# Kernel optimization log

Hardware: AMD Instinct MI355X
Metric: run time of the kernel (lower is better)

Reference implementation:

```python
import jax, jax.numpy as jnp
import numpy as np

B, S, HID = 2, 2048, 2048
H, KV, D = 16, 8, 128
EPS = 1e-6


def _rope_embeds(B, S, D):
    # standard RoPE cos/sin table, concatenated along last dim: [B, S, D]
    pos = jnp.arange(S, dtype=jnp.float32)  # same positions per batch row
    inv_freq = 1.0 / (10000.0 ** (jnp.arange(0, D // 2, dtype=jnp.float32) * (2.0 / D)))
    ang = pos[:, None] * inv_freq[None, :]  # [S, D/2]
    pe = jnp.concatenate([jnp.cos(ang), jnp.sin(ang)], axis=-1)  # [S, D]
    return jnp.broadcast_to(pe[None], (B, S, D))


def setup_inputs() -> dict:
    key = jax.random.key(0)
    ks = jax.random.split(key, 5)
    scale = 0.02
    return {
        "x": jax.random.normal(ks[0], (B, S, HID), jnp.float32),
        "pos_embeds": _rope_embeds(B, S, D),
        "q_w": jax.random.normal(ks[1], (H * D, HID), jnp.float32) * scale,
        "k_w": jax.random.normal(ks[2], (KV * D, HID), jnp.float32) * scale,
        "v_w": jax.random.normal(ks[3], (KV * D, HID), jnp.float32) * scale,
        "o_w": jax.random.normal(ks[4], (HID, H * D), jnp.float32) * scale,
        "q_norm_w": jnp.ones((D,), jnp.float32),
        "k_norm_w": jnp.ones((D,), jnp.float32),
    }


def _rmsnorm(x, w):
    var = jnp.mean(jnp.square(x), axis=-1, keepdims=True)
    return x * jax.lax.rsqrt(var + EPS) * w


def _apply_rope(x, pos_embeds):
    # x: [B, S, h, D]; pos_embeds: [B, S, D] = cat(cos, sin)
    x1, x2 = jnp.split(x, 2, axis=-1)
    cos, sin = jnp.split(pos_embeds[:, :, None, :], 2, axis=-1)
    return jnp.concatenate([x1 * cos - x2 * sin, x1 * sin + x2 * cos], axis=-1)


def reference(x, pos_embeds, q_w, k_w, v_w, o_w, q_norm_w, k_norm_w):
    b, s, _ = x.shape
    q = _apply_rope(_rmsnorm((x @ q_w.T).reshape(b, s, H, D), q_norm_w), pos_embeds)
    k = _apply_rope(_rmsnorm((x @ k_w.T).reshape(b, s, KV, D), k_norm_w), pos_embeds)
    v = (x @ v_w.T).reshape(b, s, KV, D)
    # GQA: repeat kv heads to match query heads
    rep = H // KV
    k = jnp.repeat(k, rep, axis=2)
    v = jnp.repeat(v, rep, axis=2)
    scores = jnp.einsum("bqhd,bkhd->bhqk", q, k) * (1.0 / np.sqrt(D))
    causal = jnp.tril(jnp.ones((s, s), dtype=bool))
    scores = jnp.where(causal[None, None], scores, jnp.finfo(scores.dtype).min)
    attn = jax.nn.softmax(scores, axis=-1)
    out = jnp.einsum("bhqk,bkhd->bqhd", attn, v).reshape(b, s, H * D)
    return out @ o_w.T
```

## Files before the change

### kernel.cpp

```cpp
#include <hip/hip_runtime.h>
#include <hip/hip_bf16.h>

#define BATCH 2
#define SEQ   2048
#define HID   2048
#define NH    16
#define NKV   8
#define HD    128

typedef __bf16 bf16;
typedef bf16  bf16x8  __attribute__((ext_vector_type(8)));
typedef bf16  bf16x4  __attribute__((ext_vector_type(4)));
typedef float floatx4 __attribute__((ext_vector_type(4)));

typedef __attribute__((address_space(3))) void lds_void;
typedef const __attribute__((address_space(1))) void gmem_void;

__device__ inline void async16(const void* g, void* l) {
    __builtin_amdgcn_global_load_lds((gmem_void*)g, (lds_void*)l, 16, 0, 0);
}

#define XN  8388608u
#define QWN 4194304u
#define KWN 2097152u
#define VWN 2097152u
#define OWN 4194304u

__global__ __launch_bounds__(256) void cvt_all(bf16* __restrict__ dst,
                                               const float* __restrict__ x,
                                               const float* __restrict__ qw,
                                               const float* __restrict__ kw,
                                               const float* __restrict__ vw,
                                               const float* __restrict__ ow)
{
    const int blk = blockIdx.x;
    const float* src;
    size_t off;
    if (blk < 4096)      { src = x;  off = (size_t)blk * 2048; }
    else if (blk < 6144) { src = qw; off = (size_t)(blk - 4096) * 2048; }
    else if (blk < 7168) { src = kw; off = (size_t)(blk - 6144) * 2048; }
    else if (blk < 8192) { src = vw; off = (size_t)(blk - 7168) * 2048; }
    else                 { src = ow; off = (size_t)(blk - 8192) * 2048; }

    const int t = threadIdx.x * 8;
    const float4* p = (const float4*)(src + off + t);
    float4 u0 = p[0], u1 = p[1];
    bf16x8 v;
    v[0] = (bf16)u0.x; v[1] = (bf16)u0.y; v[2] = (bf16)u0.z; v[3] = (bf16)u0.w;
    v[4] = (bf16)u1.x; v[5] = (bf16)u1.y; v[6] = (bf16)u1.z; v[7] = (bf16)u1.w;
    *(bf16x8*)(dst + (size_t)blk * 2048 + t) = v;
}

template <int AMODE, int WMODE, int CMODE>
__global__ __launch_bounds__(256) void gemm128(void* __restrict__ Cp,
                                               const void* __restrict__ Ap,
                                               const void* __restrict__ Wp,
                                               int M, int N, int K)
{
    __shared__ bf16 As[128 * 64];
    __shared__ bf16 Ws[128 * 64];

    const int tid  = threadIdx.x;
    const int wv   = tid >> 6;
    const int lane = tid & 63;
    const int quad = lane >> 4;
    const int c    = lane & 15;

    const int m0 = blockIdx.x * 128;
    const int n0 = blockIdx.y * 128;
    const int wm = (wv >> 1) * 64;
    const int wn = (wv & 1) * 64;

    const int arow = lane >> 3;
    const int acol = (lane & 7) * 8;

    floatx4 acc[4][4] = {};

    for (int k0 = 0; k0 < K; k0 += 64) {
        if constexpr (AMODE == 0) {
            const float* A = (const float*)Ap;
            #pragma unroll
            for (int it = 0; it < 4; it++) {
                int row = it * 32 + (tid >> 3);
                int col = (tid & 7) * 8;
                const float4* p = (const float4*)(A + (size_t)(m0 + row) * K + k0 + col);
                float4 u0 = p[0], u1 = p[1];
                bf16x8 v;
                v[0] = (bf16)u0.x; v[1] = (bf16)u0.y; v[2] = (bf16)u0.z; v[3] = (bf16)u0.w;
                v[4] = (bf16)u1.x; v[5] = (bf16)u1.y; v[6] = (bf16)u1.z; v[7] = (bf16)u1.w;
                *(bf16x8*)(&As[row * 64 + col]) = v;
            }
        } else {
            const bf16* A = (const bf16*)Ap;
            #pragma unroll
            for (int ch = 0; ch < 4; ch++) {
                int row = wv * 32 + ch * 8 + arow;
                async16(A + (size_t)(m0 + row) * K + k0 + acol,
                        &As[(wv * 32 + ch * 8) * 64]);
            }
        }
        if constexpr (WMODE == 0) {
            const float* W = (const float*)Wp;
            #pragma unroll
            for (int it = 0; it < 4; it++) {
                int row = it * 32 + (tid >> 3);
                int col = (tid & 7) * 8;
                const float4* p = (const float4*)(W + (size_t)(n0 + row) * K + k0 + col);
                float4 u0 = p[0], u1 = p[1];
                bf16x8 v;
                v[0] = (bf16)u0.x; v[1] = (bf16)u0.y; v[2] = (bf16)u0.z; v[3] = (bf16)u0.w;
                v[4] = (bf16)u1.x; v[5] = (bf16)u1.y; v[6] = (bf16)u1.z; v[7] = (bf16)u1.w;
                *(bf16x8*)(&Ws[row * 64 + col]) = v;
            }
        } else {
            const bf16* W = (const bf16*)Wp;
            #pragma unroll
            for (int ch = 0; ch < 4; ch++) {
                int row = wv * 32 + ch * 8 + arow;
                async16(W + (size_t)(n0 + row) * K + k0 + acol,
                        &Ws[(wv * 32 + ch * 8) * 64]);
            }
        }
        __syncthreads();

        #pragma unroll
        for (int t = 0; t < 2; t++) {
            bf16x8 af[4], bw[4];
            #pragma unroll
            for (int i = 0; i < 4; i++)
                af[i] = *(const bf16x8*)(&As[(wm + i * 16 + c) * 64 + t * 32 + quad * 8]);
            #pragma unroll
            for (int j = 0; j < 4; j++)
                bw[j] = *(const bf16x8*)(&Ws[(wn + j * 16 + c) * 64 + t * 32 + quad * 8]);
            #pragma unroll
            for (int i = 0; i < 4; i++)
                #pragma unroll
                for (int j = 0; j < 4; j++)
                    acc[i][j] = __builtin_amdgcn_mfma_f32_16x16x32_bf16(af[i], bw[j], acc[i][j], 0, 0, 0);
        }
        __syncthreads();
    }

    if constexpr (CMODE == 0) {
        float* C = (float*)Cp;
        #pragma unroll
        for (int i = 0; i < 4; i++)
            #pragma unroll
            for (int j = 0; j < 4; j++)
                #pragma unroll
                for (int r = 0; r < 4; r++) {
                    int m = m0 + wm + i * 16 + quad * 4 + r;
                    int n = n0 + wn + j * 16 + c;
                    C[(size_t)m * N + n] = acc[i][j][r];
                }
    } else if constexpr (CMODE == 1) {
        bf16* C = (bf16*)Cp;
        #pragma unroll
        for (int i = 0; i < 4; i++)
            #pragma unroll
            for (int j = 0; j < 4; j++)
                #pragma unroll
                for (int r = 0; r < 4; r++) {
                    int m = m0 + wm + i * 16 + quad * 4 + r;
                    int n = n0 + wn + j * 16 + c;
                    C[(size_t)m * N + n] = (bf16)acc[i][j][r];
                }
    } else if constexpr (CMODE == 2) {
        bf16* C = (bf16*)Cp;
        const int b = m0 >> 11;
        #pragma unroll
        for (int j = 0; j < 4; j++) {
            int n = n0 + wn + j * 16 + c;
            size_t base = ((size_t)b * N + n) * 2048;
            #pragma unroll
            for (int i = 0; i < 4; i++) {
                int s0 = (m0 & 2047) + wm + i * 16 + quad * 4;
                bf16x4 v;
                #pragma unroll
                for (int r = 0; r < 4; r++) v[r] = (bf16)acc[i][j][r];
                *(bf16x4*)(&C[base + s0]) = v;
            }
        }
    } else {
        bf16* Cq = (bf16*)Cp;
        if (n0 < 2048) {
            #pragma unroll
            for (int i = 0; i < 4; i++)
                #pragma unroll
                for (int j = 0; j < 4; j++)
                    #pragma unroll
                    for (int r = 0; r < 4; r++) {
                        int m = m0 + wm + i * 16 + quad * 4 + r;
                        int n = n0 + wn + j * 16 + c;
                        Cq[(size_t)m * 2048 + n] = (bf16)acc[i][j][r];
                    }
        } else if (n0 < 3072) {
            bf16* Ck = Cq + XN;
            #pragma unroll
            for (int i = 0; i < 4; i++)
                #pragma unroll
                for (int j = 0; j < 4; j++)
                    #pragma unroll
                    for (int r = 0; r < 4; r++) {
                        int m = m0 + wm + i * 16 + quad * 4 + r;
                        int n = n0 - 2048 + wn + j * 16 + c;
                        Ck[(size_t)m * 1024 + n] = (bf16)acc[i][j][r];
                    }
        } else {
            bf16* Cv = Cq + XN + QWN;
            const int b = m0 >> 11;
            #pragma unroll
            for (int j = 0; j < 4; j++) {
                int n = n0 - 3072 + wn + j * 16 + c;
                size_t base = ((size_t)b * 1024 + n) * 2048;
                #pragma unroll
                for (int i = 0; i < 4; i++) {
                    int s0 = (m0 & 2047) + wm + i * 16 + quad * 4;
                    bf16x4 v;
                    #pragma unroll
                    for (int r = 0; r < 4; r++) v[r] = (bf16)acc[i][j][r];
                    *(bf16x4*)(&Cv[base + s0]) = v;
                }
            }
        }
    }
}

__global__ __launch_bounds__(256) void gemm_o64(float* __restrict__ C,
                                                const bf16* __restrict__ A,
                                                const bf16* __restrict__ W,
                                                int M, int N, int K)
{
    __shared__ bf16 As[128 * 64];
    __shared__ bf16 Ws[64 * 64];

    const int tid  = threadIdx.x;
    const int wv   = tid >> 6;
    const int lane = tid & 63;
    const int quad = lane >> 4;
    const int c    = lane & 15;

    const int m0 = blockIdx.x * 128;
    const int n0 = blockIdx.y * 64;
    const int wm = (wv >> 1) * 64;
    const int wn = (wv & 1) * 32;

    const int arow = lane >> 3;
    const int acol = (lane & 7) * 8;

    floatx4 acc[4][2] = {};

    for (int k0 = 0; k0 < K; k0 += 64) {
        #pragma unroll
        for (int ch = 0; ch < 4; ch++) {
            int row = wv * 32 + ch * 8 + arow;
            async16(A + (size_t)(m0 + row) * K + k0 + acol,
                    &As[(wv * 32 + ch * 8) * 64]);
        }
        #pragma unroll
        for (int ch = 0; ch < 2; ch++) {
            int row = wv * 16 + ch * 8 + arow;
            async16(W + (size_t)(n0 + row) * K + k0 + acol,
                    &Ws[(wv * 16 + ch * 8) * 64]);
        }
        __syncthreads();

        #pragma unroll
        for (int t = 0; t < 2; t++) {
            bf16x8 af[4], bw[2];
            #pragma unroll
            for (int i = 0; i < 4; i++)
                af[i] = *(const bf16x8*)(&As[(wm + i * 16 + c) * 64 + t * 32 + quad * 8]);
            #pragma unroll
            for (int j = 0; j < 2; j++)
                bw[j] = *(const bf16x8*)(&Ws[(wn + j * 16 + c) * 64 + t * 32 + quad * 8]);
            #pragma unroll
            for (int i = 0; i < 4; i++)
                #pragma unroll
                for (int j = 0; j < 2; j++)
                    acc[i][j] = __builtin_amdgcn_mfma_f32_16x16x32_bf16(af[i], bw[j], acc[i][j], 0, 0, 0);
        }
        __syncthreads();
    }

    #pragma unroll
    for (int i = 0; i < 4; i++)
        #pragma unroll
        for (int j = 0; j < 2; j++)
            #pragma unroll
            for (int r = 0; r < 4; r++) {
                int m = m0 + wm + i * 16 + quad * 4 + r;
                int n = n0 + wn + j * 16 + c;
                C[(size_t)m * N + n] = acc[i][j][r];
            }
}

__global__ __launch_bounds__(128) void norm_rope_k(bf16* __restrict__ k,
                                                   const float* __restrict__ pe,
                                                   const float* __restrict__ knw)
{
    const int s  = blockIdx.x;
    const int hh = blockIdx.y;
    const int b  = blockIdx.z;
    const int d  = threadIdx.x;

    bf16* buf = k + (size_t)(b * SEQ + s) * 1024 + hh * HD;

    float x = (float)buf[d];
    float ss = x * x;
    #pragma unroll
    for (int m = 32; m; m >>= 1) ss += __shfl_xor(ss, m);

    __shared__ float red[2];
    __shared__ float nv[128];
    if ((d & 63) == 0) red[d >> 6] = ss;
    __syncthreads();
    float var = (red[0] + red[1]) * (1.0f / 128.0f);
    float nx = x * rsqrtf(var + 1e-6f) * knw[d];
    nv[d] = nx;
    __syncthreads();

    const float* pev = pe + ((size_t)b * SEQ + s) * HD;
    float o;
    if (d < 64) {
        o = nx * pev[d] - nv[d + 64] * pev[64 + d];
    } else {
        o = nv[d - 64] * pev[d] + nx * pev[d - 64];
    }
    buf[d] = (bf16)o;
}

__global__ __launch_bounds__(256) void fattn(bf16* __restrict__ O,
                                             const bf16* __restrict__ Q,
                                             const bf16* __restrict__ Kh,
                                             const bf16* __restrict__ Vtg,
                                             const float* __restrict__ pe,
                                             const float* __restrict__ qnw)
{
    const int h    = blockIdx.y;
    const int b    = blockIdx.z;
    const int qblk = (h & 8) ? (int)blockIdx.x
                             : ((int)gridDim.x - 1 - (int)blockIdx.x);
    const int kv   = h >> 1;

    const int tid  = threadIdx.x;
    const int wv   = tid >> 6;
    const int lane = tid & 63;
    const int quad = lane >> 4;
    const int c    = lane & 15;

    __shared__ bf16 Ks[64 * 136];
    __shared__ bf16 Vs[128 * 72];
    __shared__ bf16 Ps[4 * 16 * 72];

    const int qw = qblk * 64 + wv * 16;

    bf16x8 qf[4];
    {
        const bf16* qp = Q + (size_t)(b * SEQ + qw + c) * 2048 + h * HD + quad * 8;
        float qv[4][8];
        float ss = 0.0f;
        #pragma unroll
        for (int t = 0; t < 4; t++) {
            bf16x8 raw = *(const bf16x8*)(qp + t * 32);
            #pragma unroll
            for (int j = 0; j < 8; j++) { qv[t][j] = (float)raw[j]; ss += qv[t][j] * qv[t][j]; }
        }
        ss += __shfl_xor(ss, 16);
        ss += __shfl_xor(ss, 32);
        const float inv = rsqrtf(ss * (1.0f / 128.0f) + 1e-6f);
        const float* pev = pe + (size_t)(b * SEQ + qw + c) * HD + quad * 8;
        float nx[4][8], pv[4][8];
        #pragma unroll
        for (int t = 0; t < 4; t++)
            #pragma unroll
            for (int j = 0; j < 8; j++) {
                pv[t][j] = pev[t * 32 + j];
                nx[t][j] = qv[t][j] * inv * qnw[t * 32 + quad * 8 + j];
            }
        #pragma unroll
        for (int t = 0; t < 2; t++)
            #pragma unroll
            for (int j = 0; j < 8; j++) {
                qf[t][j]     = (bf16)(nx[t][j] * pv[t][j]     - nx[t + 2][j] * pv[t + 2][j]);
                qf[t + 2][j] = (bf16)(nx[t][j] * pv[t + 2][j] + nx[t + 2][j] * pv[t][j]);
            }
    }

    floatx4 o_acc[8] = {};
    float l_part[4] = {};

    const bf16* kbase = Kh  + (size_t)b * SEQ * 1024 + kv * HD;
    const bf16* vbase = Vtg + ((size_t)b * 1024 + kv * HD) * 2048;

    const int kr  = tid >> 2, ksc = (tid & 3) * 32;
    const int vd  = tid >> 1, vkc = (tid & 1) * 32;
    bf16* psw = &Ps[wv * 16 * 72];
    const int nkt = qblk + 1;
    const float kS = 0.08838834764831845f * 1.4426950408889634f;
    const float kB = 11.5f * 1.4426950408889634f;

    bf16x8 kreg[4], vreg[4];
    {
        const bf16* kp = kbase + (size_t)kr * 1024 + ksc;
        const bf16* vp = vbase + (size_t)vd * 2048 + vkc;
        #pragma unroll
        for (int i = 0; i < 4; i++) kreg[i] = *(const bf16x8*)(kp + i * 8);
        #pragma unroll
        for (int i = 0; i < 4; i++) vreg[i] = *(const bf16x8*)(vp + i * 8);
    }

    for (int kt = 0; kt < nkt; kt++) {
        const int k0 = kt * 64;
        #pragma unroll
        for (int i = 0; i < 4; i++)
            *(bf16x8*)(&Ks[kr * 136 + ksc + i * 8]) = kreg[i];
        #pragma unroll
        for (int i = 0; i < 4; i++)
            *(bf16x8*)(&Vs[vd * 72 + vkc + i * 8]) = vreg[i];
        __syncthreads();

        if (kt + 1 < nkt) {
            const bf16* kp = kbase + (size_t)(k0 + 64 + kr) * 1024 + ksc;
            const bf16* vp = vbase + (size_t)vd * 2048 + (k0 + 64) + vkc;
            #pragma unroll
            for (int i = 0; i < 4; i++) kreg[i] = *(const bf16x8*)(kp + i * 8);
            #pragma unroll
            for (int i = 0; i < 4; i++) vreg[i] = *(const bf16x8*)(vp + i * 8);
        }

        floatx4 sc[4] = {};
        #pragma unroll
        for (int t = 0; t < 4; t++) {
            #pragma unroll
            for (int g = 0; g < 4; g++) {
                bf16x8 kf = *(const bf16x8*)(&Ks[(g * 16 + c) * 136 + t * 32 + quad * 8]);
                sc[g] = __builtin_amdgcn_mfma_f32_16x16x32_bf16(qf[t], kf, sc[g], 0, 0, 0);
            }
        }

        const bool last = (kt == nkt - 1);
        #pragma unroll
        for (int r = 0; r < 4; r++) {
            const int qrow = qw + quad * 4 + r;
            #pragma unroll
            for (int g = 0; g < 4; g++) {
                float p = exp2f(sc[g][r] * kS - kB);
                if (last && (k0 + g * 16 + c > qrow)) p = 0.0f;
                l_part[r] += p;
                psw[(quad * 4 + r) * 72 + g * 16 + c] = (bf16)p;
            }
        }
        asm volatile("s_waitcnt lgkmcnt(0)" ::: "memory");
        bf16x8 pf0 = *(const bf16x8*)(&psw[c * 72 + quad * 8]);
        bf16x8 pf1 = *(const bf16x8*)(&psw[c * 72 + 32 + quad * 8]);

        #pragma unroll
        for (int f = 0; f < 8; f++) {
            bf16x8 vf0 = *(const bf16x8*)(&Vs[(f * 16 + c) * 72 + quad * 8]);
            bf16x8 vf1 = *(const bf16x8*)(&Vs[(f * 16 + c) * 72 + 32 + quad * 8]);
            o_acc[f] = __builtin_amdgcn_mfma_f32_16x16x32_bf16(pf0, vf0, o_acc[f], 0, 0, 0);
            o_acc[f] = __builtin_amdgcn_mfma_f32_16x16x32_bf16(pf1, vf1, o_acc[f], 0, 0, 0);
        }
        __syncthreads();
    }

    #pragma unroll
    for (int r = 0; r < 4; r++) {
        float l = l_part[r];
        #pragma unroll
        for (int msk = 8; msk; msk >>= 1) l += __shfl_xor(l, msk);
        const float inv = 1.0f / l;
        bf16* op = O + (size_t)(b * SEQ + qw + quad * 4 + r) * 2048 + h * HD;
        #pragma unroll
        for (int f = 0; f < 8; f++) op[f * 16 + c] = (bf16)(o_acc[f][r] * inv);
    }
}

extern "C" void kernel_launch(void* const* d_in, const int* in_sizes, int n_in,
                              void* d_out, int out_size, void* d_ws, size_t ws_size,
                              hipStream_t stream)
{
    const float* x   = (const float*)d_in[0];
    const float* pe  = (const float*)d_in[1];
    const float* qw  = (const float*)d_in[2];
    const float* kw  = (const float*)d_in[3];
    const float* vw  = (const float*)d_in[4];
    const float* ow  = (const float*)d_in[5];
    const float* qnw = (const float*)d_in[6];
    const float* knw = (const float*)d_in[7];
    float* out = (float*)d_out;

    bf16* qb = (bf16*)d_ws;
    bf16* kb = qb + XN;
    bf16* vt = kb + KWN * 2;
    bf16* ab = vt + VWN * 2;
    bf16* cvt_base = ab + XN;

    const bool fit = ws_size >= (size_t)92274688;
    const int M = BATCH * SEQ;

    if (fit) {
        bf16* xb  = cvt_base;
        bf16* qwb = xb  + XN;
        bf16* owb = qwb + QWN + KWN + VWN;

        cvt_all<<<10240, 256, 0, stream>>>(xb, x, qw, kw, vw, ow);

        gemm128<1, 1, 3><<<dim3(32, 32), 256, 0, stream>>>(qb, xb, qwb, M, 4096, 2048);

        norm_rope_k<<<dim3(SEQ, NKV, BATCH), 128, 0, stream>>>(kb, pe, knw);
        fattn<<<dim3(SEQ / 64, NH, BATCH), 256, 0, stream>>>(ab, qb, kb, vt, pe, qnw);

        gemm_o64<<<dim3(32, 32), 256, 0, stream>>>(out, ab, owb, M, 2048, 2048);
    } else {
        gemm128<0, 0, 1><<<dim3(32, 16), 256, 0, stream>>>(qb, x, qw, M, 2048, 2048);
        gemm128<0, 0, 1><<<dim3(32,  8), 256, 0, stream>>>(kb, x, kw, M, 1024, 2048);
        gemm128<0, 0, 2><<<dim3(32,  8), 256, 0, stream>>>(vt, x, vw, M, 1024, 2048);

        norm_rope_k<<<dim3(SEQ, NKV, BATCH), 128, 0, stream>>>(kb, pe, knw);
        fattn<<<dim3(SEQ / 64, NH, BATCH), 256, 0, stream>>>(ab, qb, kb, vt, pe, qnw);

        gemm128<0, 0, 0><<<dim3(32, 16), 256, 0, stream>>>(out, ab, ow, M, 2048, 2048);
    }
}
```

Baseline: 402.5 us.

## Process 128 query rows per attention block to reuse K/V tiles

Each attention workgroup now covers 128 query rows instead of 64, with every wave handling two 16-row query sub-blocks against the same K/V tiles staged in LDS. This halves the number of K/V tile loads per query row and doubles the MFMA work per synchronisation. The P scratch buffer is resized with a padded stride, and causal masking is applied over the last two key tiles. The cost is higher register pressure from doubled accumulators, possibly lower occupancy, half as many workgroups, and more wasted masked work in the diagonal tiles.

```diff
diff --git a/kernel.cpp b/kernel.cpp
--- a/kernel.cpp
+++ b/kernel.cpp
@@ -351,13 +351,14 @@
 
     __shared__ bf16 Ks[64 * 136];
     __shared__ bf16 Vs[128 * 72];
-    __shared__ bf16 Ps[4 * 16 * 72];
-
-    const int qw = qblk * 64 + wv * 16;
-
-    bf16x8 qf[4];
-    {
-        const bf16* qp = Q + (size_t)(b * SEQ + qw + c) * 2048 + h * HD + quad * 8;
+    __shared__ bf16 Ps[4 * 32 * 76];
+
+    const int qw = qblk * 128 + wv * 32;
+
+    bf16x8 qf[2][4];
+    #pragma unroll
+    for (int ib = 0; ib < 2; ib++) {
+        const bf16* qp = Q + (size_t)(b * SEQ + qw + ib * 16 + c) * 2048 + h * HD + quad * 8;
         float qv[4][8];
         float ss = 0.0f;
         #pragma unroll
@@ -369,7 +370,7 @@
         ss += __shfl_xor(ss, 16);
         ss += __shfl_xor(ss, 32);
         const float inv = rsqrtf(ss * (1.0f / 128.0f) + 1e-6f);
-        const float* pev = pe + (size_t)(b * SEQ + qw + c) * HD + quad * 8;
+        const float* pev = pe + (size_t)(b * SEQ + qw + ib * 16 + c) * HD + quad * 8;
         float nx[4][8], pv[4][8];
         #pragma unroll
         for (int t = 0; t < 4; t++)
@@ -382,21 +383,21 @@
         for (int t = 0; t < 2; t++)
             #pragma unroll
             for (int j = 0; j < 8; j++) {
-                qf[t][j]     = (bf16)(nx[t][j] * pv[t][j]     - nx[t + 2][j] * pv[t + 2][j]);
-                qf[t + 2][j] = (bf16)(nx[t][j] * pv[t + 2][j] + nx[t + 2][j] * pv[t][j]);
-            }
-    }
-
-    floatx4 o_acc[8] = {};
-    float l_part[4] = {};
+                qf[ib][t][j]     = (bf16)(nx[t][j] * pv[t][j]     - nx[t + 2][j] * pv[t + 2][j]);
+                qf[ib][t + 2][j] = (bf16)(nx[t][j] * pv[t + 2][j] + nx[t + 2][j] * pv[t][j]);
+            }
+    }
+
+    floatx4 o_acc[2][8] = {};
+    float l_part[2][4] = {};
 
     const bf16* kbase = Kh  + (size_t)b * SEQ * 1024 + kv * HD;
     const bf16* vbase = Vtg + ((size_t)b * 1024 + kv * HD) * 2048;
 
     const int kr  = tid >> 2, ksc = (tid & 3) * 32;
     const int vd  = tid >> 1, vkc = (tid & 1) * 32;
-    bf16* psw = &Ps[wv * 16 * 72];
-    const int nkt = qblk + 1;
+    bf16* psw = &Ps[wv * 32 * 76];
+    const int nkt = 2 * qblk + 2;
     const float kS = 0.08838834764831845f * 1.4426950408889634f;
     const float kB = 11.5f * 1.4426950408889634f;
 
@@ -429,51 +430,67 @@
             for (int i = 0; i < 4; i++) vreg[i] = *(const bf16x8*)(vp + i * 8);
         }
 
-        floatx4 sc[4] = {};
+        floatx4 sc0[4] = {}, sc1[4] = {};
         #pragma unroll
         for (int t = 0; t < 4; t++) {
             #pragma unroll
             for (int g = 0; g < 4; g++) {
                 bf16x8 kf = *(const bf16x8*)(&Ks[(g * 16 + c) * 136 + t * 32 + quad * 8]);
-                sc[g] = __builtin_amdgcn_mfma_f32_16x16x32_bf16(qf[t], kf, sc[g], 0, 0, 0);
-            }
-        }
-
-        const bool last = (kt == nkt - 1);
+                sc0[g] = __builtin_amdgcn_mfma_f32_16x16x32_bf16(qf[0][t], kf, sc0[g], 0, 0, 0);
+                sc1[g] = __builtin_amdgcn_mfma_f32_16x16x32_bf16(qf[1][t], kf, sc1[g], 0, 0, 0);
+            }
+        }
+
+        const bool tail = (kt >= nkt - 2);
         #pragma unroll
         for (int r = 0; r < 4; r++) {
-            const int qrow = qw + quad * 4 + r;
+            const int qrow0 = qw + quad * 4 + r;
+            const int qrow1 = qrow0 + 16;
             #pragma unroll
             for (int g = 0; g < 4; g++) {
-                float p = exp2f(sc[g][r] * kS - kB);
-                if (last && (k0 + g * 16 + c > qrow)) p = 0.0f;
-                l_part[r] += p;
-                psw[(quad * 4 + r) * 72 + g * 16 + c] = (bf16)p;
+                float p0 = exp2f(sc0[g][r] * kS - kB);
+                float p1 = exp2f(sc1[g][r] * kS - kB);
+                if (tail) {
+                    const int key = k0 + g * 16 + c;
+                    if (key > qrow0) p0 = 0.0f;
+                    if (key > qrow1) p1 = 0.0f;
+                }
+                l_part[0][r] += p0;
+                l_part[1][r] += p1;
+                psw[(quad * 4 + r) * 76 + g * 16 + c]        = (bf16)p0;
+                psw[(16 + quad * 4 + r) * 76 + g * 16 + c]   = (bf16)p1;
             }
         }
         asm volatile("s_waitcnt lgkmcnt(0)" ::: "memory");
-        bf16x8 pf0 = *(const bf16x8*)(&psw[c * 72 + quad * 8]);
-        bf16x8 pf1 = *(const bf16x8*)(&psw[c * 72 + 32 + quad * 8]);
+        bf16x8 pf00 = *(const bf16x8*)(&psw[c * 76 + quad * 8]);
+        bf16x8 pf01 = *(const bf16x8*)(&psw[c * 76 + 32 + quad * 8]);
+        bf16x8 pf10 = *(const bf16x8*)(&psw[(16 + c) * 76 + quad * 8]);
+        bf16x8 pf11 = *(const bf16x8*)(&psw[(16 + c) * 76 + 32 + quad * 8]);
 
         #pragma unroll
         for (int f = 0; f < 8; f++) {
             bf16x8 vf0 = *(const bf16x8*)(&Vs[(f * 16 + c) * 72 + quad * 8]);
             bf16x8 vf1 = *(const bf16x8*)(&Vs[(f * 16 + c) * 72 + 32 + quad * 8]);
-            o_acc[f] = __builtin_amdgcn_mfma_f32_16x16x32_bf16(pf0, vf0, o_acc[f], 0, 0, 0);
-            o_acc[f] = __builtin_amdgcn_mfma_f32_16x16x32_bf16(pf1, vf1, o_acc[f], 0, 0, 0);
+            o_acc[0][f] = __builtin_amdgcn_mfma_f32_16x16x32_bf16(pf00, vf0, o_acc[0][f], 0, 0, 0);
+            o_acc[0][f] = __builtin_amdgcn_mfma_f32_16x16x32_bf16(pf01, vf1, o_acc[0][f], 0, 0, 0);
+            o_acc[1][f] = __builtin_amdgcn_mfma_f32_16x16x32_bf16(pf10, vf0, o_acc[1][f], 0, 0, 0);
+            o_acc[1][f] = __builtin_amdgcn_mfma_f32_16x16x32_bf16(pf11, vf1, o_acc[1][f], 0, 0, 0);
         }
         __syncthreads();
     }
 
     #pragma unroll
-    for (int r = 0; r < 4; r++) {
-        float l = l_part[r];
-        #pragma unroll
-        for (int msk = 8; msk; msk >>= 1) l += __shfl_xor(l, msk);
-        const float inv = 1.0f / l;
-        bf16* op = O + (size_t)(b * SEQ + qw + quad * 4 + r) * 2048 + h * HD;
-        #pragma unroll
-        for (int f = 0; f < 8; f++) op[f * 16 + c] = (bf16)(o_acc[f][r] * inv);
+    for (int ib = 0; ib < 2; ib++) {
+        #pragma unroll
+        for (int r = 0; r < 4; r++) {
+            float l = l_part[ib][r];
+            #pragma unroll
+            for (int msk = 8; msk; msk >>= 1) l += __shfl_xor(l, msk);
+            const float inv = 1.0f / l;
+            bf16* op = O + (size_t)(b * SEQ + qw + ib * 16 + quad * 4 + r) * 2048 + h * HD;
+            #pragma unroll
+            for (int f = 0; f < 8; f++) op[f * 16 + c] = (bf16)(o_acc[ib][f][r] * inv);
+        }
     }
 }
 
@@ -510,7 +527,7 @@
         gemm128<1, 1, 3><<<dim3(32, 32), 256, 0, stream>>>(qb, xb, qwb, M, 4096, 2048);
 
         norm_rope_k<<<dim3(SEQ, NKV, BATCH), 128, 0, stream>>>(kb, pe, knw);
-        fattn<<<dim3(SEQ / 64, NH, BATCH), 256, 0, stream>>>(ab, qb, kb, vt, pe, qnw);
+        fattn<<<dim3(SEQ / 128, NH, BATCH), 256, 0, stream>>>(ab, qb, kb, vt, pe, qnw);
 
         gemm_o64<<<dim3(32, 32), 256, 0, stream>>>(out, ab, owb, M, 2048, 2048);
     } else {
@@ -519,7 +536,7 @@
         gemm128<0, 0, 2><<<dim3(32,  8), 256, 0, stream>>>(vt, x, vw, M, 1024, 2048);
 
         norm_rope_k<<<dim3(SEQ, NKV, BATCH), 128, 0, stream>>>(kb, pe, knw);
-        fattn<<<dim3(SEQ / 64, NH, BATCH), 256, 0, stream>>>(ab, qb, kb, vt, pe, qnw);
+        fattn<<<dim3(SEQ / 128, NH, BATCH), 256, 0, stream>>>(ab, qb, kb, vt, pe, qnw);
 
         gemm128<0, 0, 0><<<dim3(32, 16), 256, 0, stream>>>(out, ab, ow, M, 2048, 2048);
     }
```

Result: slower. 440.4 us (+9.4%).
